# Kernel tuning notes

Measured on AMD Instinct MI355X. Metric: run time of the kernel, lower is better.

## Reference

```python
import jax, jax.numpy as jnp
import numpy as np

N_NODES = 50000
N_EDGES = 600000
D_IN = 128
D_OUT = 128
N_BASES = 4
N_RATINGS = 5


def setup_inputs() -> dict:
    key = jax.random.key(0)
    k1, k2, k3, k4, k5, k6 = jax.random.split(key, 6)
    x = jax.random.normal(k1, (N_NODES, D_IN), dtype=jnp.float32)
    edge_index = jax.random.randint(k2, (2, N_EDGES), 0, N_NODES, dtype=jnp.int64)
    edge_type = jax.random.randint(k3, (N_EDGES,), 0, N_RATINGS, dtype=jnp.int64)
    # basis matrices B_k: (out, in); a_r stacked over ratings: (R, K); W_0: (out, in)
    B = jax.random.normal(k4, (N_BASES, D_OUT, D_IN), dtype=jnp.float32) * 0.05
    A = jax.random.normal(k5, (N_RATINGS, N_BASES), dtype=jnp.float32) * 0.05
    W0 = jax.random.normal(k6, (D_OUT, D_IN), dtype=jnp.float32) * 0.05
    return {"x": x, "edge_index": edge_index, "edge_type": edge_type, "B": B, "A": A, "W0": W0}


def reference(x, edge_index, edge_type, B, A, W0):
    # self-loop term: (W0 @ x^T)^T == x @ W0^T
    n_nodes = x.shape[0]
    src, tgt = edge_index[0], edge_index[1]
    out = x @ W0.T  # [N, out]
    # per-relation basis-composed weights W_r = sum_k a_r[k] * B_k  -> [R, out, in]
    W = jnp.einsum('rk,kod->rod', A, B)
    n_ratings = A.shape[0]
    for r in range(n_ratings):  # small fixed relation set
        h = x @ W[r].T                     # [N, out] transform once per node
        msg = jnp.where((edge_type == r)[:, None], h[src], jnp.float32(0))  # [E, out]
        out = out + jax.ops.segment_sum(msg, tgt, num_segments=n_nodes)
    return out
```

## Files before the change

### kernel.cpp

```cpp
#include <hip/hip_runtime.h>

#define N_NODES 50000
#define N_EDGES 600000
#define D 128
#define KTOT 768
#define NB_SCAN 196

typedef __attribute__((ext_vector_type(8))) short short8;
typedef __attribute__((ext_vector_type(4))) float float4v;

static __device__ __forceinline__ float bf2f(unsigned int u16) {
    union { unsigned int i; float f; } v; v.i = u16 << 16; return v.f;
}
static __device__ __forceinline__ unsigned short f2bf(float f) {
    union { float f; unsigned int i; } v; v.f = f;
    unsigned int u = v.i;
    return (unsigned short)((u + 0x7FFFu + ((u >> 16) & 1u)) >> 16);
}
static __device__ __forceinline__ float h2f(unsigned int h) {
    unsigned int s = (h >> 15) & 1u, e = (h >> 10) & 0x1fu, m = h & 0x3ffu;
    unsigned int bits = (e == 0) ? (s << 31)
                                 : ((s << 31) | ((e + 112u) << 23) | (m << 13));
    union { unsigned int i; float f; } v; v.i = bits; return v.f;
}

__global__ __launch_bounds__(256) void setup(int* __restrict__ flags,
                                             int* __restrict__ cnt) {
    int i = blockIdx.x * 256 + threadIdx.x;
    if (i < N_NODES) cnt[i] = 0;
    if (i < 8) flags[i] = 0;
}

__global__ __launch_bounds__(256) void detect_all(const int* __restrict__ ei,
                                                  const int* __restrict__ et,
                                                  const unsigned int* __restrict__ x,
                                                  const unsigned int* __restrict__ B,
                                                  const unsigned int* __restrict__ A,
                                                  const unsigned int* __restrict__ W0,
                                                  int* __restrict__ flags) {
    __shared__ int sflag;
    if (threadIdx.x == 0) sflag = 0;
    __syncthreads();
    int b = blockIdx.x, acc = 0, fidx;
    if (b < 192) {
        fidx = 0;
        for (int i = b * 256 + threadIdx.x; i < N_EDGES; i += 192 * 256)
            acc |= ei[2 * i + 1];
    } else if (b < 240) {
        fidx = 1;
        for (int i = (b - 192) * 256 + threadIdx.x; i < N_EDGES / 2; i += 48 * 256)
            acc |= et[2 * i + 1];
    } else if (b < 288) {
        fidx = 2;
        for (int i = (b - 240) * 256 + threadIdx.x; i < 600000; i += 48 * 256) {
            unsigned int e = (x[i] >> 7) & 0xffu;
            acc |= (e > 0xA0u || e < 0x50u) ? 1 : 0;
        }
    } else if (b < 300) {
        fidx = 3;
        for (int i = (b - 288) * 256 + threadIdx.x; i < 32768; i += 12 * 256) {
            unsigned int e = (B[i] >> 7) & 0xffu;
            acc |= (e > 0xA0u || e < 0x50u) ? 1 : 0;
        }
    } else if (b == 300) {
        fidx = 4;
        for (int i = threadIdx.x; i < 10; i += 256) {
            unsigned int e = (A[i] >> 7) & 0xffu;
            acc |= (e > 0xA0u || e < 0x50u) ? 1 : 0;
        }
    } else if (b < 307) {
        fidx = 5;
        for (int i = (b - 301) * 256 + threadIdx.x; i < 8192; i += 6 * 256) {
            unsigned int e = (W0[i] >> 7) & 0xffu;
            acc |= (e > 0xA0u || e < 0x50u) ? 1 : 0;
        }
    } else {
        fidx = 6;
        for (int i = (b - 307) * 256 + threadIdx.x; i < 300000; i += 48 * 256) {
            unsigned int el = (x[i] >> 7) & 0xffu, eh = (x[i] >> 23) & 0xffu;
            acc |= (el < 0x58u || eh < 0x58u) ? 1 : 0;
        }
    }
    if (acc) sflag = 1;
    __syncthreads();
    if (threadIdx.x == 0 && sflag) atomicOr(flags + fidx, 1);
}

static __device__ __forceinline__ float loadw(const void* p, int idx, int f32) {
    return f32 ? ((const float*)p)[idx] : bf2f(((const unsigned short*)p)[idx]);
}

__global__ __launch_bounds__(256) void norm_hist_prep(const int* __restrict__ ei,
                                                      const int* __restrict__ et,
                                                      int* __restrict__ idx32,
                                                      int* __restrict__ et32,
                                                      int* __restrict__ cnt,
                                                      const void* __restrict__ A,
                                                      const void* __restrict__ B,
                                                      const void* __restrict__ W0,
                                                      unsigned short* __restrict__ wcatB,
                                                      const int* __restrict__ flags) {
    int b = blockIdx.x;
    if (b < 4688) {
        int i = b * 256 + threadIdx.x;
        if (i < 2 * N_EDGES) {
            int v = flags[0] ? ei[i] : ei[2 * i];
            idx32[i] = v;
            if (i >= N_EDGES && (unsigned)v < (unsigned)N_NODES)
                atomicAdd(&cnt[v], 1);
        }
    } else if (b < 7032) {
        int i = (b - 4688) * 256 + threadIdx.x;
        if (i < N_EDGES) et32[i] = flags[1] ? et[i] : et[2 * i];
    } else {
        int idx = (b - 7032) * 256 + threadIdx.x;
        int fB = flags[3], fA = flags[4], fW = flags[5];
        int o = idx / KTOT, k = idx % KTOT;
        float v;
        if (k < D) {
            v = loadw(W0, o * D + k, fW);
        } else {
            int r = (k - D) >> 7, d = (k - D) & 127;
            v = 0.f;
#pragma unroll
            for (int j = 0; j < 4; ++j)
                v += loadw(A, r * 4 + j, fA) * loadw(B, (j * D + o) * D + d, fB);
        }
        wcatB[idx] = f2bf(v);
    }
}

__global__ __launch_bounds__(256) void prep_wt6_direct(const void* __restrict__ A,
                                                       const void* __restrict__ B,
                                                       const void* __restrict__ W0,
                                                       float* __restrict__ wcatT6F,
                                                       const int* __restrict__ flags) {
    int idx = blockIdx.x * 256 + threadIdx.x;
    int fB = flags[3], fA = flags[4], fW = flags[5];
    int slot = idx >> 14, d = (idx >> 7) & 127, o = idx & 127;
    float v;
    if (slot == 0) {
        v = loadw(W0, o * D + d, fW);
    } else {
        int r = slot - 1;
        v = 0.f;
#pragma unroll
        for (int j = 0; j < 4; ++j)
            v += loadw(A, r * 4 + j, fA) * loadw(B, (j * D + o) * D + d, fB);
    }
    wcatT6F[idx] = v;
}

__global__ __launch_bounds__(256) void scan1(const int* __restrict__ cnt,
                                             int* __restrict__ bsum) {
    __shared__ int sh[256];
    int t = threadIdx.x, idx = blockIdx.x * 256 + t;
    sh[t] = (idx < N_NODES) ? cnt[idx] : 0;
    __syncthreads();
    for (int off = 128; off > 0; off >>= 1) {
        if (t < off) sh[t] += sh[t + off];
        __syncthreads();
    }
    if (t == 0) bsum[blockIdx.x] = sh[0];
}

__global__ __launch_bounds__(256) void scan2(const int* __restrict__ bsum,
                                             int* __restrict__ bscan,
                                             int* __restrict__ offsets) {
    __shared__ int sh[256];
    int t = threadIdx.x;
    int v = (t < NB_SCAN) ? bsum[t] : 0;
    sh[t] = v;
    __syncthreads();
    for (int off = 1; off < 256; off <<= 1) {
        int a = (t >= off) ? sh[t - off] : 0;
        __syncthreads();
        sh[t] += a;
        __syncthreads();
    }
    if (t < NB_SCAN) bscan[t] = sh[t] - v;
    if (t == 255) offsets[N_NODES] = sh[255];
}

__global__ __launch_bounds__(256) void scan3(const int* __restrict__ cnt,
                                             const int* __restrict__ bscan,
                                             int* __restrict__ offsets,
                                             int* __restrict__ cursor) {
    __shared__ int sh[256];
    int t = threadIdx.x, idx = blockIdx.x * 256 + t;
    int v = (idx < N_NODES) ? cnt[idx] : 0;
    sh[t] = v;
    __syncthreads();
    for (int off = 1; off < 256; off <<= 1) {
        int a = (t >= off) ? sh[t - off] : 0;
        __syncthreads();
        sh[t] += a;
        __syncthreads();
    }
    if (idx < N_NODES) {
        int excl = sh[t] - v + bscan[blockIdx.x];
        offsets[idx] = excl;
        cursor[idx] = excl;
    }
}

__global__ __launch_bounds__(256) void place(const int* __restrict__ src,
                                             const int* __restrict__ tgt,
                                             const int* __restrict__ et,
                                             int* __restrict__ cursor,
                                             int* __restrict__ entries) {
    int e = blockIdx.x * 256 + threadIdx.x;
    if (e >= N_EDGES) return;
    int s = src[e], g = tgt[e], r = et[e];
    if ((unsigned)s >= (unsigned)N_NODES || (unsigned)g >= (unsigned)N_NODES || (unsigned)r >= 5u) return;
    int pos = atomicAdd(&cursor[g], 1);
    entries[pos] = s * 8 + r;
}

__global__ __launch_bounds__(256) void conv_x(const void* __restrict__ xraw,
                                              unsigned short* __restrict__ Xcat,
                                              const int* __restrict__ flags) {
    int idx = blockIdx.x * 256 + threadIdx.x;
    int n = idx >> 5, cg = idx & 31;
    int f32 = flags[2], f16 = flags[6];
    unsigned short o0, o1, o2, o3;
    if (f32) {
        float4 v = *((const float4*)xraw + idx);
        o0 = f2bf(v.x); o1 = f2bf(v.y); o2 = f2bf(v.z); o3 = f2bf(v.w);
    } else {
        uint2 v = *((const uint2*)xraw + idx);
        if (f16) {
            o0 = f2bf(h2f(v.x & 0xffffu)); o1 = f2bf(h2f(v.x >> 16));
            o2 = f2bf(h2f(v.y & 0xffffu)); o3 = f2bf(h2f(v.y >> 16));
        } else {
            o0 = v.x & 0xffffu; o1 = v.x >> 16; o2 = v.y & 0xffffu; o3 = v.y >> 16;
        }
    }
    unsigned long long pack = (unsigned long long)o0 | ((unsigned long long)o1 << 16) |
                              ((unsigned long long)o2 << 32) | ((unsigned long long)o3 << 48);
    *(unsigned long long*)(Xcat + (size_t)n * KTOT + cg * 4) = pack;
}

#define AGG_ACC2(ent, xw)                                            \
    {                                                                \
        int r_ = (ent) & 7;                                          \
        float flo_ = __uint_as_float((xw) << 16);                    \
        float fhi_ = __uint_as_float((xw) & 0xffff0000u);            \
        if (r_ == 0)      { a0 += flo_; a1 += fhi_; }                \
        else if (r_ == 1) { b0 += flo_; b1 += fhi_; }                \
        else if (r_ == 2) { c0 += flo_; c1 += fhi_; }                \
        else if (r_ == 3) { d0 += flo_; d1 += fhi_; }                \
        else              { e0 += flo_; e1 += fhi_; }                \
    }

static __device__ __forceinline__ unsigned int agg_row_load(
        const unsigned int* __restrict__ Xcat32, int ent, int lane) {
    unsigned int row = (unsigned int)(ent >> 3);
    if (row >= (unsigned)N_NODES) row = 0u;
    return Xcat32[(size_t)row * 384 + lane];
}

__global__ __launch_bounds__(256) void aggregate(const int* __restrict__ offsets,
                                                 const int* __restrict__ entries,
                                                 unsigned int* __restrict__ Xcat32) {
    int tid = threadIdx.x;
    int wid = tid >> 6, lane = tid & 63;
    int n = __builtin_amdgcn_readfirstlane(blockIdx.x * 4 + wid);
    int beg = __builtin_amdgcn_readfirstlane(offsets[n]);
    int end = __builtin_amdgcn_readfirstlane(offsets[n + 1]);
    float a0 = 0, a1 = 0, b0 = 0, b1 = 0, c0 = 0, c1 = 0, d0 = 0, d1 = 0, e0 = 0, e1 = 0;

    for (int base = beg; base < end; base += 64) {
        int cnt = end - base;
        if (cnt > 64) cnt = 64;
        int eload = entries[base + lane];
        int j = 0;
        for (; j + 3 < cnt; j += 4) {
            int en0 = __builtin_amdgcn_readlane(eload, j);
            int en1 = __builtin_amdgcn_readlane(eload, j + 1);
            int en2 = __builtin_amdgcn_readlane(eload, j + 2);
            int en3 = __builtin_amdgcn_readlane(eload, j + 3);
            unsigned int x0 = agg_row_load(Xcat32, en0, lane);
            unsigned int x1 = agg_row_load(Xcat32, en1, lane);
            unsigned int x2 = agg_row_load(Xcat32, en2, lane);
            unsigned int x3 = agg_row_load(Xcat32, en3, lane);
            AGG_ACC2(en0, x0);
            AGG_ACC2(en1, x1);
            AGG_ACC2(en2, x2);
            AGG_ACC2(en3, x3);
        }
        for (; j < cnt; ++j) {
            int en = __builtin_amdgcn_readlane(eload, j);
            unsigned int xw = agg_row_load(Xcat32, en, lane);
            AGG_ACC2(en, xw);
        }
    }

    size_t o = (size_t)n * 384 + 64 + lane;
    Xcat32[o]       = (unsigned int)f2bf(a0) | ((unsigned int)f2bf(a1) << 16);
    Xcat32[o + 64]  = (unsigned int)f2bf(b0) | ((unsigned int)f2bf(b1) << 16);
    Xcat32[o + 128] = (unsigned int)f2bf(c0) | ((unsigned int)f2bf(c1) << 16);
    Xcat32[o + 192] = (unsigned int)f2bf(d0) | ((unsigned int)f2bf(d1) << 16);
    Xcat32[o + 256] = (unsigned int)f2bf(e0) | ((unsigned int)f2bf(e1) << 16);
}

__global__ __launch_bounds__(256) void gemm_mfma(const unsigned short* __restrict__ Xcat,
                                                 const unsigned short* __restrict__ wcatB,
                                                 float* __restrict__ outF) {
    __shared__ unsigned short xs[64 * 72];
    __shared__ unsigned short wsd[128 * 72];
    int tid = threadIdx.x;
    int m0 = blockIdx.x * 64;
    int wid = tid >> 6, lane = tid & 63;
    int wm = (wid & 1) * 32, wn = (wid >> 1) * 64;
    int lm = lane & 15, kg = lane >> 4;

    float4v accf[2][4];
#pragma unroll
    for (int i = 0; i < 2; ++i)
#pragma unroll
        for (int j = 0; j < 4; ++j) accf[i][j] = (float4v){0.f, 0.f, 0.f, 0.f};

    for (int kc = 0; kc < 12; ++kc) {
        if (kc) __syncthreads();
#pragma unroll
        for (int i = 0; i < 2; ++i) {
            int c = tid + i * 256;
            int row = c >> 3, col = (c & 7) * 8;
            int gm = m0 + row;
            short8 xv = {0, 0, 0, 0, 0, 0, 0, 0};
            if (gm < N_NODES)
                xv = *(const short8*)(Xcat + (size_t)gm * KTOT + kc * 64 + col);
            *(short8*)(&xs[row * 72 + col]) = xv;
        }
#pragma unroll
        for (int i = 0; i < 4; ++i) {
            int c = tid + i * 256;
            int row = c >> 3, col = (c & 7) * 8;
            short8 wv = *(const short8*)(wcatB + (size_t)row * KTOT + kc * 64 + col);
            *(short8*)(&wsd[row * 72 + col]) = wv;
        }
        __syncthreads();
#pragma unroll
        for (int kb = 0; kb < 2; ++kb) {
            int k = kb * 32 + kg * 8;
            short8 a[2], b[4];
#pragma unroll
            for (int i = 0; i < 2; ++i)
                a[i] = *(const short8*)(&xs[(wm + i * 16 + lm) * 72 + k]);
#pragma unroll
            for (int j = 0; j < 4; ++j)
                b[j] = *(const short8*)(&wsd[(wn + j * 16 + lm) * 72 + k]);
#pragma unroll
            for (int i = 0; i < 2; ++i)
#pragma unroll
                for (int j = 0; j < 4; ++j)
                    accf[i][j] = __builtin_amdgcn_mfma_f32_16x16x32_bf16(a[i], b[j], accf[i][j], 0, 0, 0);
        }
    }

#pragma unroll
    for (int i = 0; i < 2; ++i) {
        int gmb = m0 + wm + i * 16 + kg * 4;
#pragma unroll
        for (int j = 0; j < 4; ++j) {
            int gn = wn + j * 16 + lm;
#pragma unroll
            for (int r = 0; r < 4; ++r) {
                int gm = gmb + r;
                if (gm < N_NODES) outF[(size_t)gm * D + gn] = accf[i][j][r];
            }
        }
    }
}

static __device__ __forceinline__ float2 readx2(const void* x, int node, int lane,
                                                int f32, int f16) {
    if (f32) return *((const float2*)x + (size_t)node * 64 + lane);
    unsigned int w = *((const unsigned int*)x + (size_t)node * 64 + lane);
    float2 r;
    if (f16) { r.x = h2f(w & 0xffffu); r.y = h2f(w >> 16); }
    else     { r.x = bf2f(w & 0xffffu); r.y = bf2f(w >> 16); }
    return r;
}

__global__ __launch_bounds__(256) void self_raw(const void* __restrict__ x,
                                                const float* __restrict__ wcatT6F,
                                                float* __restrict__ outF,
                                                const int* __restrict__ flags) {
    int t = blockIdx.x * 256 + threadIdx.x;
    int n = t >> 6, lane = t & 63;
    int f32 = flags[2], f16 = flags[6];
    float2 xp = readx2(x, n, lane, f32, f16);
    float m0 = 0.f, m1 = 0.f;
#pragma unroll 8
    for (int dp = 0; dp < 64; ++dp) {
        float xa = __shfl(xp.x, dp);
        float xc = __shfl(xp.y, dp);
        float2 w0 = *(const float2*)(wcatT6F + (size_t)(2 * dp) * D + 2 * lane);
        float2 w1 = *(const float2*)(wcatT6F + (size_t)(2 * dp + 1) * D + 2 * lane);
        m0 += xa * w0.x + xc * w1.x;
        m1 += xa * w0.y + xc * w1.y;
    }
    *((float2*)outF + (size_t)n * 64 + lane) = make_float2(m0, m1);
}

__global__ __launch_bounds__(256) void edge_raw(const int* __restrict__ src,
                                                const int* __restrict__ tgt,
                                                const int* __restrict__ et,
                                                const void* __restrict__ x,
                                                const float* __restrict__ wcatT6F,
                                                float* __restrict__ outF,
                                                const int* __restrict__ flags) {
    int t = blockIdx.x * 256 + threadIdx.x;
    int e = t >> 6, lane = t & 63;
    if (e >= N_EDGES) return;
    int f32 = flags[2], f16 = flags[6];
    int s = src[e], g = tgt[e], r = et[e];
    if ((unsigned)s >= (unsigned)N_NODES || (unsigned)g >= (unsigned)N_NODES || (unsigned)r >= 5u) return;
    float2 xp = readx2(x, s, lane, f32, f16);
    const float* wt = wcatT6F + (size_t)(1 + r) * D * D;
    float m0 = 0.f, m1 = 0.f;
#pragma unroll 8
    for (int dp = 0; dp < 64; ++dp) {
        float xa = __shfl(xp.x, dp);
        float xc = __shfl(xp.y, dp);
        float2 w0 = *(const float2*)(wt + (size_t)(2 * dp) * D + 2 * lane);
        float2 w1 = *(const float2*)(wt + (size_t)(2 * dp + 1) * D + 2 * lane);
        m0 += xa * w0.x + xc * w1.x;
        m1 += xa * w0.y + xc * w1.y;
    }
    float* ap = outF + (size_t)g * D + lane * 2;
    atomicAdd(ap + 0, m0);
    atomicAdd(ap + 1, m1);
}

extern "C" void kernel_launch(void* const* d_in, const int* in_sizes, int n_in,
                              void* d_out, int out_size, void* d_ws, size_t ws_size,
                              hipStream_t stream) {
    const void* x  = nullptr; const int* ei = nullptr; const int* et = nullptr;
    const void* B  = nullptr; const void* A = nullptr; const void* W0 = nullptr;
    for (int i = 0; i < n_in; ++i) {
        switch (in_sizes[i]) {
            case 6400000: x  = d_in[i]; break;
            case 1200000: ei = (const int*)d_in[i]; break;
            case 600000:  et = (const int*)d_in[i]; break;
            case 65536:   B  = d_in[i]; break;
            case 20:      A  = d_in[i]; break;
            case 16384:   W0 = d_in[i]; break;
            default: break;
        }
    }
    if (!x || !ei || !et || !B || !A || !W0) {
        x  = d_in[0]; ei = (const int*)d_in[1]; et = (const int*)d_in[2];
        B  = d_in[3]; A  = d_in[4]; W0 = d_in[5];
    }
    float* outF = (float*)d_out;

    char* ws = (char*)d_ws;
    int*   flags   = (int*)(ws + 0);
    float* wcatT6F = (float*)(ws + 256);
    unsigned short* wcatB = (unsigned short*)(ws + 393472);
    int* offsets  = (int*)(ws + 590080);
    int* cursor   = (int*)(ws + 790144);
    int* cnt      = (int*)(ws + 990144);
    int* bsum     = (int*)(ws + 1190144);
    int* bscan    = (int*)(ws + 1191168);
    int* entries  = (int*)(ws + 1192192);
    int* idx32    = (int*)(ws + 3592192);
    int* et32     = (int*)(ws + 8392192);
    unsigned short* Xcat = (unsigned short*)(ws + 3592192);
    const size_t needMain = 3592192ull + 76800000ull;
    const size_t needT3   = 393472ull;

    int* src32 = idx32;
    int* tgt32 = idx32 + N_EDGES;

    setup<<<NB_SCAN, 256, 0, stream>>>(flags, cnt);
    detect_all<<<355, 256, 0, stream>>>(ei, et, (const unsigned int*)x,
                                        (const unsigned int*)B, (const unsigned int*)A,
                                        (const unsigned int*)W0, flags);

    if (ws_size >= needMain) {
        norm_hist_prep<<<7416, 256, 0, stream>>>(ei, et, idx32, et32, cnt,
                                                 A, B, W0, wcatB, flags);
        scan1<<<NB_SCAN, 256, 0, stream>>>(cnt, bsum);
        scan2<<<1, 256, 0, stream>>>(bsum, bscan, offsets);
        scan3<<<NB_SCAN, 256, 0, stream>>>(cnt, bscan, offsets, cursor);
        place<<<2344, 256, 0, stream>>>(src32, tgt32, et32, cursor, entries);
        conv_x<<<6250, 256, 0, stream>>>(x, Xcat, flags);
        aggregate<<<12500, 256, 0, stream>>>(offsets, entries, (unsigned int*)Xcat);
        gemm_mfma<<<782, 256, 0, stream>>>(Xcat, wcatB, outF);
    } else if (ws_size >= needT3) {
        prep_wt6_direct<<<384, 256, 0, stream>>>(A, B, W0, wcatT6F, flags);
        self_raw<<<12500, 256, 0, stream>>>(x, wcatT6F, outF, flags);
        edge_raw<<<150000, 256, 0, stream>>>(ei, ei + N_EDGES, et, x, wcatT6F, outF, flags);
    }
}
```

Measured before the change: 232.5 us.

## Fuse x conversion into prep, single-pass scan, and enlarge pipelined GEMM tile

Folds the x-to-bf16 conversion into the edge-normalisation/histogram kernel, relocating Xcat so it no longer aliases idx32. Replaces the three-kernel scan with a single decoupled-lookback scan that uses ticket-ordered block IDs. Doubles the GEMM M-tile to 128 rows and register-prefetches the next K chunk while the current one computes. The aim is fewer launches and better GEMM reuse, at the cost of a larger workspace requirement, spin-waiting in the scan, and higher register pressure in the GEMM.

```diff
diff --git a/kernel.cpp b/kernel.cpp
--- a/kernel.cpp
+++ b/kernel.cpp
@@ -25,10 +25,12 @@
 }
 
 __global__ __launch_bounds__(256) void setup(int* __restrict__ flags,
-                                             int* __restrict__ cnt) {
+                                             int* __restrict__ cnt,
+                                             unsigned int* __restrict__ scanst) {
     int i = blockIdx.x * 256 + threadIdx.x;
     if (i < N_NODES) cnt[i] = 0;
     if (i < 8) flags[i] = 0;
+    if (i < 200) scanst[i] = 0;
 }
 
 __global__ __launch_bounds__(256) void detect_all(const int* __restrict__ ei,
@@ -90,7 +92,7 @@
     return f32 ? ((const float*)p)[idx] : bf2f(((const unsigned short*)p)[idx]);
 }
 
-__global__ __launch_bounds__(256) void norm_hist_prep(const int* __restrict__ ei,
+__global__ __launch_bounds__(256) void norm_hist_conv(const int* __restrict__ ei,
                                                       const int* __restrict__ et,
                                                       int* __restrict__ idx32,
                                                       int* __restrict__ et32,
@@ -99,6 +101,8 @@
                                                       const void* __restrict__ B,
                                                       const void* __restrict__ W0,
                                                       unsigned short* __restrict__ wcatB,
+                                                      const void* __restrict__ xraw,
+                                                      unsigned short* __restrict__ Xcat,
                                                       const int* __restrict__ flags) {
     int b = blockIdx.x;
     if (b < 4688) {
@@ -112,7 +116,7 @@
     } else if (b < 7032) {
         int i = (b - 4688) * 256 + threadIdx.x;
         if (i < N_EDGES) et32[i] = flags[1] ? et[i] : et[2 * i];
-    } else {
+    } else if (b < 7416) {
         int idx = (b - 7032) * 256 + threadIdx.x;
         int fB = flags[3], fA = flags[4], fW = flags[5];
         int o = idx / KTOT, k = idx % KTOT;
@@ -127,6 +131,26 @@
                 v += loadw(A, r * 4 + j, fA) * loadw(B, (j * D + o) * D + d, fB);
         }
         wcatB[idx] = f2bf(v);
+    } else {
+        int idx = (b - 7416) * 256 + threadIdx.x;
+        int n = idx >> 5, cg = idx & 31;
+        int f32 = flags[2], f16 = flags[6];
+        unsigned short o0, o1, o2, o3;
+        if (f32) {
+            float4 v = *((const float4*)xraw + idx);
+            o0 = f2bf(v.x); o1 = f2bf(v.y); o2 = f2bf(v.z); o3 = f2bf(v.w);
+        } else {
+            uint2 v = *((const uint2*)xraw + idx);
+            if (f16) {
+                o0 = f2bf(h2f(v.x & 0xffffu)); o1 = f2bf(h2f(v.x >> 16));
+                o2 = f2bf(h2f(v.y & 0xffffu)); o3 = f2bf(h2f(v.y >> 16));
+            } else {
+                o0 = v.x & 0xffffu; o1 = v.x >> 16; o2 = v.y & 0xffffu; o3 = v.y >> 16;
+            }
+        }
+        unsigned long long pack = (unsigned long long)o0 | ((unsigned long long)o1 << 16) |
+                                  ((unsigned long long)o2 << 32) | ((unsigned long long)o3 << 48);
+        *(unsigned long long*)(Xcat + (size_t)n * KTOT + cg * 4) = pack;
     }
 }
 
@@ -151,43 +175,21 @@
     wcatT6F[idx] = v;
 }
 
-__global__ __launch_bounds__(256) void scan1(const int* __restrict__ cnt,
-                                             int* __restrict__ bsum) {
+#define SC_AGG (1u << 30)
+#define SC_PRE (1u << 31)
+__global__ __launch_bounds__(256) void scan_fused(const int* __restrict__ cnt,
+                                                  int* __restrict__ offsets,
+                                                  int* __restrict__ cursor,
+                                                  unsigned int* __restrict__ scanst) {
     __shared__ int sh[256];
-    int t = threadIdx.x, idx = blockIdx.x * 256 + t;
-    sh[t] = (idx < N_NODES) ? cnt[idx] : 0;
+    __shared__ int sbid, sprefix;
+    unsigned int* status = scanst;
+    unsigned int* ticket = scanst + 196;
+    int t = threadIdx.x;
+    if (t == 0) sbid = (int)atomicAdd(ticket, 1u);
     __syncthreads();
-    for (int off = 128; off > 0; off >>= 1) {
-        if (t < off) sh[t] += sh[t + off];
-        __syncthreads();
-    }
-    if (t == 0) bsum[blockIdx.x] = sh[0];
-}
-
-__global__ __launch_bounds__(256) void scan2(const int* __restrict__ bsum,
-                                             int* __restrict__ bscan,
-                                             int* __restrict__ offsets) {
-    __shared__ int sh[256];
-    int t = threadIdx.x;
-    int v = (t < NB_SCAN) ? bsum[t] : 0;
-    sh[t] = v;
-    __syncthreads();
-    for (int off = 1; off < 256; off <<= 1) {
-        int a = (t >= off) ? sh[t - off] : 0;
-        __syncthreads();
-        sh[t] += a;
-        __syncthreads();
-    }
-    if (t < NB_SCAN) bscan[t] = sh[t] - v;
-    if (t == 255) offsets[N_NODES] = sh[255];
-}
-
-__global__ __launch_bounds__(256) void scan3(const int* __restrict__ cnt,
-                                             const int* __restrict__ bscan,
-                                             int* __restrict__ offsets,
-                                             int* __restrict__ cursor) {
-    __shared__ int sh[256];
-    int t = threadIdx.x, idx = blockIdx.x * 256 + t;
+    int bid = sbid;
+    int idx = bid * 256 + t;
     int v = (idx < N_NODES) ? cnt[idx] : 0;
     sh[t] = v;
     __syncthreads();
@@ -197,10 +199,25 @@
         sh[t] += a;
         __syncthreads();
     }
+    if (t == 0) {
+        int total = sh[255];
+        atomicExch(&status[bid], (unsigned int)total | SC_AGG);
+        int prefix = 0;
+        for (int j = bid - 1; j >= 0; --j) {
+            unsigned int s;
+            do { s = atomicAdd(&status[j], 0u); } while ((s & (SC_AGG | SC_PRE)) == 0u);
+            prefix += (int)(s & 0x3FFFFFFFu);
+            if (s & SC_PRE) break;
+        }
+        atomicExch(&status[bid], (unsigned int)(prefix + total) | SC_PRE);
+        sprefix = prefix;
+    }
+    __syncthreads();
+    int excl = sh[t] - v + sprefix;
     if (idx < N_NODES) {
-        int excl = sh[t] - v + bscan[blockIdx.x];
         offsets[idx] = excl;
         cursor[idx] = excl;
+        if (idx == N_NODES - 1) offsets[N_NODES] = excl + v;
     }
 }
 
@@ -215,30 +232,6 @@
     if ((unsigned)s >= (unsigned)N_NODES || (unsigned)g >= (unsigned)N_NODES || (unsigned)r >= 5u) return;
     int pos = atomicAdd(&cursor[g], 1);
     entries[pos] = s * 8 + r;
-}
-
-__global__ __launch_bounds__(256) void conv_x(const void* __restrict__ xraw,
-                                              unsigned short* __restrict__ Xcat,
-                                              const int* __restrict__ flags) {
-    int idx = blockIdx.x * 256 + threadIdx.x;
-    int n = idx >> 5, cg = idx & 31;
-    int f32 = flags[2], f16 = flags[6];
-    unsigned short o0, o1, o2, o3;
-    if (f32) {
-        float4 v = *((const float4*)xraw + idx);
-        o0 = f2bf(v.x); o1 = f2bf(v.y); o2 = f2bf(v.z); o3 = f2bf(v.w);
-    } else {
-        uint2 v = *((const uint2*)xraw + idx);
-        if (f16) {
-            o0 = f2bf(h2f(v.x & 0xffffu)); o1 = f2bf(h2f(v.x >> 16));
-            o2 = f2bf(h2f(v.y & 0xffffu)); o3 = f2bf(h2f(v.y >> 16));
-        } else {
-            o0 = v.x & 0xffffu; o1 = v.x >> 16; o2 = v.y & 0xffffu; o3 = v.y >> 16;
-        }
-    }
-    unsigned long long pack = (unsigned long long)o0 | ((unsigned long long)o1 << 16) |
-                              ((unsigned long long)o2 << 32) | ((unsigned long long)o3 << 48);
-    *(unsigned long long*)(Xcat + (size_t)n * KTOT + cg * 4) = pack;
 }
 
 #define AGG_ACC2(ent, xw)                                            \
@@ -307,52 +300,62 @@
 __global__ __launch_bounds__(256) void gemm_mfma(const unsigned short* __restrict__ Xcat,
                                                  const unsigned short* __restrict__ wcatB,
                                                  float* __restrict__ outF) {
-    __shared__ unsigned short xs[64 * 72];
+    __shared__ unsigned short xs[128 * 72];
     __shared__ unsigned short wsd[128 * 72];
     int tid = threadIdx.x;
-    int m0 = blockIdx.x * 64;
+    int m0 = blockIdx.x * 128;
     int wid = tid >> 6, lane = tid & 63;
-    int wm = (wid & 1) * 32, wn = (wid >> 1) * 64;
+    int wm = (wid & 1) * 64, wn = (wid >> 1) * 64;
     int lm = lane & 15, kg = lane >> 4;
-
-    float4v accf[2][4];
-#pragma unroll
-    for (int i = 0; i < 2; ++i)
+    int srow = tid >> 3, scol = (tid & 7) * 8;
+
+    float4v accf[4][4];
+#pragma unroll
+    for (int i = 0; i < 4; ++i)
 #pragma unroll
         for (int j = 0; j < 4; ++j) accf[i][j] = (float4v){0.f, 0.f, 0.f, 0.f};
+
+    short8 xr[4], wr[4];
+    const short8 z8 = {0, 0, 0, 0, 0, 0, 0, 0};
+#pragma unroll
+    for (int i = 0; i < 4; ++i) {
+        int row = srow + i * 32;
+        int gm = m0 + row;
+        xr[i] = (gm < N_NODES) ? *(const short8*)(Xcat + (size_t)gm * KTOT + scol) : z8;
+        wr[i] = *(const short8*)(wcatB + (size_t)row * KTOT + scol);
+    }
 
     for (int kc = 0; kc < 12; ++kc) {
         if (kc) __syncthreads();
 #pragma unroll
-        for (int i = 0; i < 2; ++i) {
-            int c = tid + i * 256;
-            int row = c >> 3, col = (c & 7) * 8;
-            int gm = m0 + row;
-            short8 xv = {0, 0, 0, 0, 0, 0, 0, 0};
-            if (gm < N_NODES)
-                xv = *(const short8*)(Xcat + (size_t)gm * KTOT + kc * 64 + col);
-            *(short8*)(&xs[row * 72 + col]) = xv;
-        }
-#pragma unroll
         for (int i = 0; i < 4; ++i) {
-            int c = tid + i * 256;
-            int row = c >> 3, col = (c & 7) * 8;
-            short8 wv = *(const short8*)(wcatB + (size_t)row * KTOT + kc * 64 + col);
-            *(short8*)(&wsd[row * 72 + col]) = wv;
+            int row = srow + i * 32;
+            *(short8*)(&xs[row * 72 + scol]) = xr[i];
+            *(short8*)(&wsd[row * 72 + scol]) = wr[i];
         }
         __syncthreads();
+        if (kc + 1 < 12) {
+            int kb = (kc + 1) * 64 + scol;
+#pragma unroll
+            for (int i = 0; i < 4; ++i) {
+                int row = srow + i * 32;
+                int gm = m0 + row;
+                xr[i] = (gm < N_NODES) ? *(const short8*)(Xcat + (size_t)gm * KTOT + kb) : z8;
+                wr[i] = *(const short8*)(wcatB + (size_t)row * KTOT + kb);
+            }
+        }
 #pragma unroll
         for (int kb = 0; kb < 2; ++kb) {
             int k = kb * 32 + kg * 8;
-            short8 a[2], b[4];
-#pragma unroll
-            for (int i = 0; i < 2; ++i)
+            short8 a[4], b[4];
+#pragma unroll
+            for (int i = 0; i < 4; ++i)
                 a[i] = *(const short8*)(&xs[(wm + i * 16 + lm) * 72 + k]);
 #pragma unroll
             for (int j = 0; j < 4; ++j)
                 b[j] = *(const short8*)(&wsd[(wn + j * 16 + lm) * 72 + k]);
 #pragma unroll
-            for (int i = 0; i < 2; ++i)
+            for (int i = 0; i < 4; ++i)
 #pragma unroll
                 for (int j = 0; j < 4; ++j)
                     accf[i][j] = __builtin_amdgcn_mfma_f32_16x16x32_bf16(a[i], b[j], accf[i][j], 0, 0, 0);
@@ -360,7 +363,7 @@
     }
 
 #pragma unroll
-    for (int i = 0; i < 2; ++i) {
+    for (int i = 0; i < 4; ++i) {
         int gmb = m0 + wm + i * 16 + kg * 4;
 #pragma unroll
         for (int j = 0; j < 4; ++j) {
@@ -464,33 +467,29 @@
     int* offsets  = (int*)(ws + 590080);
     int* cursor   = (int*)(ws + 790144);
     int* cnt      = (int*)(ws + 990144);
-    int* bsum     = (int*)(ws + 1190144);
-    int* bscan    = (int*)(ws + 1191168);
-    int* entries  = (int*)(ws + 1192192);
-    int* idx32    = (int*)(ws + 3592192);
-    int* et32     = (int*)(ws + 8392192);
-    unsigned short* Xcat = (unsigned short*)(ws + 3592192);
-    const size_t needMain = 3592192ull + 76800000ull;
+    unsigned int* scanst = (unsigned int*)(ws + 1190144);
+    int* entries  = (int*)(ws + 1191168);
+    int* idx32    = (int*)(ws + 3591168);
+    int* et32     = (int*)(ws + 8391168);
+    unsigned short* Xcat = (unsigned short*)(ws + 10791168);
+    const size_t needMain = 10791168ull + 76800000ull;
     const size_t needT3   = 393472ull;
 
     int* src32 = idx32;
     int* tgt32 = idx32 + N_EDGES;
 
-    setup<<<NB_SCAN, 256, 0, stream>>>(flags, cnt);
+    setup<<<NB_SCAN, 256, 0, stream>>>(flags, cnt, scanst);
     detect_all<<<355, 256, 0, stream>>>(ei, et, (const unsigned int*)x,
                                         (const unsigned int*)B, (const unsigned int*)A,
                                         (const unsigned int*)W0, flags);
 
     if (ws_size >= needMain) {
-        norm_hist_prep<<<7416, 256, 0, stream>>>(ei, et, idx32, et32, cnt,
-                                                 A, B, W0, wcatB, flags);
-        scan1<<<NB_SCAN, 256, 0, stream>>>(cnt, bsum);
-        scan2<<<1, 256, 0, stream>>>(bsum, bscan, offsets);
-        scan3<<<NB_SCAN, 256, 0, stream>>>(cnt, bscan, offsets, cursor);
+        norm_hist_conv<<<13666, 256, 0, stream>>>(ei, et, idx32, et32, cnt,
+                                                  A, B, W0, wcatB, x, Xcat, flags);
+        scan_fused<<<NB_SCAN, 256, 0, stream>>>(cnt, offsets, cursor, scanst);
         place<<<2344, 256, 0, stream>>>(src32, tgt32, et32, cursor, entries);
-        conv_x<<<6250, 256, 0, stream>>>(x, Xcat, flags);
         aggregate<<<12500, 256, 0, stream>>>(offsets, entries, (unsigned int*)Xcat);
-        gemm_mfma<<<782, 256, 0, stream>>>(Xcat, wcatB, outF);
+        gemm_mfma<<<391, 256, 0, stream>>>(Xcat, wcatB, outF);
     } else if (ws_size >= needT3) {
         prep_wt6_direct<<<384, 256, 0, stream>>>(A, B, W0, wcatT6F, flags);
         self_raw<<<12500, 256, 0, stream>>>(x, wcatT6F, outF, flags);
```

Measured after the change: 228.5 us (median of 3 runs). About the same (-1.7%).
